# Performance work log

Measured on AMD Instinct MI355X. Metric: run time of the kernel, lower is better.

The kernel has to match this reference:

```python
import jax, jax.numpy as jnp
import numpy as np

N, D = 512, 256
NUM_CLASSES = 10
MARGIN = 1.0


def setup_inputs() -> dict:
    key = jax.random.key(0)
    k1, k2 = jax.random.split(key)
    embeddings = jax.random.normal(k1, (N, D), dtype=jnp.float32)
    labels = jax.random.randint(k2, (N,), 0, NUM_CLASSES, dtype=jnp.int32)
    return {"embeddings": embeddings, "labels": labels}


def _pairwise_euclidean(e):
    # dist[i, j] = sqrt(sum((e_i - e_j)^2)), computed via the Gram matrix.
    sq = jnp.sum(e * e, axis=-1)                       # [N]
    d2 = sq[:, None] + sq[None, :] - 2.0 * (e @ e.T)   # [N, N]
    d2 = jnp.maximum(d2, 0.0)
    # safe sqrt: zero-distance pairs (diagonal) get dist 0 with no NaN grads
    pos = d2 > 0
    return jnp.where(pos, jnp.sqrt(jnp.where(pos, d2, 1.0)), 0.0)


def reference(embeddings, labels):
    n = labels.shape[0]
    dist = _pairwise_euclidean(embeddings)             # [N, N]

    same = labels[:, None] == labels[None, :]          # [N, N]
    not_self = ~jnp.eye(n, dtype=bool)
    pos_mask = same & not_self                         # valid (anchor, positive)
    neg_mask = ~same                                   # valid (anchor, negative)

    # triplet (a, p, n): relu(d_ap - d_an + margin)
    tl = jax.nn.relu(dist[:, :, None] - dist[:, None, :] + MARGIN)  # [N, N, N]
    valid = pos_mask[:, :, None] & neg_mask[:, None, :]             # [N, N, N]

    loss_sum = jnp.sum(jnp.where(valid, tl, 0.0))
    # use_gt_than_zero_mean=False: divide by total number of valid triplets
    count = jnp.sum(valid).astype(embeddings.dtype)
    return loss_sum / count
```

## Files before the change

kernel.cpp:

```cpp
#include <hip/hip_runtime.h>

#define NN 512
#define DD 256
#define MARGIN 1.0f

__global__ __launch_bounds__(256) void triplet_partial(
    const float* __restrict__ e, const int* __restrict__ labels,
    float* __restrict__ partial, int* __restrict__ pcount)
{
    const int a    = blockIdx.x;
    const int t    = threadIdx.x;
    const int lane = t & 63;
    const int wave = t >> 6;

    __shared__ __align__(16) float ea[DD];
    __shared__ int   slab[NN];
    __shared__ float plist[NN];
    __shared__ float nlist[NN];
    __shared__ int   segP[8], segN[8];
    __shared__ float red[4];

    ea[t] = e[(size_t)a * DD + t];
    slab[t]       = labels[t];
    slab[t + 256] = labels[t + 256];
    __syncthreads();

    const int la = slab[a];

    float acc0 = 0.f, acc1 = 0.f;
    const float4* r0 = reinterpret_cast<const float4*>(e + (size_t)t * DD);
    const float4* r1 = reinterpret_cast<const float4*>(e + (size_t)(t + 256) * DD);
    #pragma unroll 4
    for (int k = 0; k < DD / 4; ++k) {
        float4 v0 = r0[k];
        float4 v1 = r1[k];
        float4 ev = *reinterpret_cast<const float4*>(&ea[k * 4]);
        float d;
        d = ev.x - v0.x; acc0 = fmaf(d, d, acc0);
        d = ev.y - v0.y; acc0 = fmaf(d, d, acc0);
        d = ev.z - v0.z; acc0 = fmaf(d, d, acc0);
        d = ev.w - v0.w; acc0 = fmaf(d, d, acc0);
        d = ev.x - v1.x; acc1 = fmaf(d, d, acc1);
        d = ev.y - v1.y; acc1 = fmaf(d, d, acc1);
        d = ev.z - v1.z; acc1 = fmaf(d, d, acc1);
        d = ev.w - v1.w; acc1 = fmaf(d, d, acc1);
    }
    const float d0 = sqrtf(acc0);
    const float d1 = sqrtf(acc1);

    const int l0 = slab[t];
    const int l1 = slab[t + 256];
    const bool vp0 = (l0 == la) && (t != a);
    const bool vp1 = (l1 == la) && (t + 256 != a);
    const bool vn0 = (l0 != la);
    const bool vn1 = (l1 != la);

    const unsigned long long mp0 = __ballot(vp0);
    const unsigned long long mp1 = __ballot(vp1);
    const unsigned long long mn0 = __ballot(vn0);
    const unsigned long long mn1 = __ballot(vn1);

    if (lane == 0) {
        segP[wave]     = __popcll(mp0);
        segP[4 + wave] = __popcll(mp1);
        segN[wave]     = __popcll(mn0);
        segN[4 + wave] = __popcll(mn1);
    }
    __syncthreads();

    int baseP0 = 0, baseP1 = 0, baseN0 = 0, baseN1 = 0, totP = 0, totN = 0;
    #pragma unroll
    for (int s = 0; s < 8; ++s) {
        const int vP = segP[s], vN = segN[s];
        totP += vP; totN += vN;
        if (s < wave)     { baseP0 += vP; baseN0 += vN; }
        if (s < 4 + wave) { baseP1 += vP; baseN1 += vN; }
    }

    const unsigned long long lower = (lane == 0) ? 0ull : ((~0ull) >> (64 - lane));
    if (vp0) plist[baseP0 + __popcll(mp0 & lower)] = d0 + MARGIN;
    if (vp1) plist[baseP1 + __popcll(mp1 & lower)] = d1 + MARGIN;
    if (vn0) nlist[baseN0 + __popcll(mn0 & lower)] = d0;
    if (vn1) nlist[baseN1 + __popcll(mn1 & lower)] = d1;
    __syncthreads();

    float sum = 0.f;
    for (int p = wave; p < totP; p += 4) {
        const float dpm = plist[p];
        for (int n = lane; n < totN; n += 64) {
            const float v = dpm - nlist[n];
            sum += fmaxf(v, 0.f);
        }
    }

    #pragma unroll
    for (int off = 32; off > 0; off >>= 1) sum += __shfl_down(sum, off);
    if (lane == 0) red[wave] = sum;
    __syncthreads();
    if (t == 0) {
        partial[a] = red[0] + red[1] + red[2] + red[3];
        pcount[a]  = totP * totN;
    }
}

__global__ __launch_bounds__(256) void reduce_final(
    const float* __restrict__ partial, const int* __restrict__ pcount,
    float* __restrict__ out)
{
    const int t = threadIdx.x;
    double s = 0.0;
    long long c = 0;
    for (int i = t; i < NN; i += 256) { s += (double)partial[i]; c += (long long)pcount[i]; }
    __shared__ double sd[256];
    __shared__ long long sc[256];
    sd[t] = s; sc[t] = c;
    __syncthreads();
    for (int off = 128; off > 0; off >>= 1) {
        if (t < off) { sd[t] += sd[t + off]; sc[t] += sc[t + off]; }
        __syncthreads();
    }
    if (t == 0) out[0] = (float)(sd[0] / (double)sc[0]);
}

extern "C" void kernel_launch(void* const* d_in, const int* in_sizes, int n_in,
                              void* d_out, int out_size, void* d_ws, size_t ws_size,
                              hipStream_t stream) {
    const float* e      = (const float*)d_in[0];
    const int*   labels = (const int*)d_in[1];
    float* out     = (float*)d_out;
    float* partial = (float*)d_ws;
    int*   pcount  = (int*)((char*)d_ws + NN * sizeof(float));

    triplet_partial<<<NN, 256, 0, stream>>>(e, labels, partial, pcount);
    reduce_final<<<1, 256, 0, stream>>>(partial, pcount, out);
}
```

Before: 92.07 us.

## Split distance computation into tiled kernel and fuse final reduction via atomics

Moves the pairwise distance computation into its own kernel in which each block computes four anchor rows against 256 columns. Each loaded embedding row is now reused across four anchors, cutting the redundant global traffic where every anchor block re-read the whole embedding matrix. The pair-counting kernel reads the precomputed distances from a workspace buffer. The separate reduction kernel is replaced by float and int atomics plus a last-block ticket that writes the output, which makes the float summation order nondeterministic and the count an int that could overflow for larger sizes.

```diff
diff --git a/kernel.cpp b/kernel.cpp
--- a/kernel.cpp
+++ b/kernel.cpp
@@ -4,49 +4,72 @@
 #define DD 256
 #define MARGIN 1.0f
 
-__global__ __launch_bounds__(256) void triplet_partial(
-    const float* __restrict__ e, const int* __restrict__ labels,
-    float* __restrict__ partial, int* __restrict__ pcount)
+__global__ __launch_bounds__(256) void dist_kernel(
+    const float* __restrict__ e, float* __restrict__ dist,
+    float* __restrict__ gsum, int* __restrict__ gcnt, int* __restrict__ gdone)
+{
+    const int g = blockIdx.x >> 1;
+    const int h = blockIdx.x & 1;
+    const int t = threadIdx.x;
+    const int j = h * 256 + t;
+    const int a0 = g * 4;
+
+    if (blockIdx.x == 0 && t == 0) { *gsum = 0.f; *gcnt = 0; *gdone = 0; }
+
+    __shared__ __align__(16) float eas[DD][4];
+
+    #pragma unroll
+    for (int ai = 0; ai < 4; ++ai)
+        eas[t][ai] = e[(size_t)(a0 + ai) * DD + t];
+    __syncthreads();
+
+    float acc0 = 0.f, acc1 = 0.f, acc2 = 0.f, acc3 = 0.f;
+    const float4* rowj = reinterpret_cast<const float4*>(e + (size_t)j * DD);
+
+    #pragma unroll 4
+    for (int kb = 0; kb < DD / 4; ++kb) {
+        const float4 v = rowj[kb];
+        const float vv[4] = {v.x, v.y, v.z, v.w};
+        #pragma unroll
+        for (int q = 0; q < 4; ++q) {
+            const float4 av = *reinterpret_cast<const float4*>(&eas[kb * 4 + q][0]);
+            float d;
+            d = av.x - vv[q]; acc0 = fmaf(d, d, acc0);
+            d = av.y - vv[q]; acc1 = fmaf(d, d, acc1);
+            d = av.z - vv[q]; acc2 = fmaf(d, d, acc2);
+            d = av.w - vv[q]; acc3 = fmaf(d, d, acc3);
+        }
+    }
+
+    dist[(size_t)(a0 + 0) * NN + j] = sqrtf(acc0);
+    dist[(size_t)(a0 + 1) * NN + j] = sqrtf(acc1);
+    dist[(size_t)(a0 + 2) * NN + j] = sqrtf(acc2);
+    dist[(size_t)(a0 + 3) * NN + j] = sqrtf(acc3);
+}
+
+__global__ __launch_bounds__(256) void pairs_kernel(
+    const float* __restrict__ dist, const int* __restrict__ labels,
+    float* __restrict__ gsum, int* __restrict__ gcnt, int* __restrict__ gdone,
+    float* __restrict__ out)
 {
     const int a    = blockIdx.x;
     const int t    = threadIdx.x;
     const int lane = t & 63;
     const int wave = t >> 6;
 
-    __shared__ __align__(16) float ea[DD];
     __shared__ int   slab[NN];
     __shared__ float plist[NN];
     __shared__ float nlist[NN];
     __shared__ int   segP[8], segN[8];
     __shared__ float red[4];
 
-    ea[t] = e[(size_t)a * DD + t];
     slab[t]       = labels[t];
     slab[t + 256] = labels[t + 256];
     __syncthreads();
 
     const int la = slab[a];
-
-    float acc0 = 0.f, acc1 = 0.f;
-    const float4* r0 = reinterpret_cast<const float4*>(e + (size_t)t * DD);
-    const float4* r1 = reinterpret_cast<const float4*>(e + (size_t)(t + 256) * DD);
-    #pragma unroll 4
-    for (int k = 0; k < DD / 4; ++k) {
-        float4 v0 = r0[k];
-        float4 v1 = r1[k];
-        float4 ev = *reinterpret_cast<const float4*>(&ea[k * 4]);
-        float d;
-        d = ev.x - v0.x; acc0 = fmaf(d, d, acc0);
-        d = ev.y - v0.y; acc0 = fmaf(d, d, acc0);
-        d = ev.z - v0.z; acc0 = fmaf(d, d, acc0);
-        d = ev.w - v0.w; acc0 = fmaf(d, d, acc0);
-        d = ev.x - v1.x; acc1 = fmaf(d, d, acc1);
-        d = ev.y - v1.y; acc1 = fmaf(d, d, acc1);
-        d = ev.z - v1.z; acc1 = fmaf(d, d, acc1);
-        d = ev.w - v1.w; acc1 = fmaf(d, d, acc1);
-    }
-    const float d0 = sqrtf(acc0);
-    const float d1 = sqrtf(acc1);
+    const float d0 = dist[(size_t)a * NN + t];
+    const float d1 = dist[(size_t)a * NN + t + 256];
 
     const int l0 = slab[t];
     const int l1 = slab[t + 256];
@@ -97,29 +120,18 @@
     for (int off = 32; off > 0; off >>= 1) sum += __shfl_down(sum, off);
     if (lane == 0) red[wave] = sum;
     __syncthreads();
+
     if (t == 0) {
-        partial[a] = red[0] + red[1] + red[2] + red[3];
-        pcount[a]  = totP * totN;
+        atomicAdd(gsum, red[0] + red[1] + red[2] + red[3]);
+        atomicAdd(gcnt, totP * totN);
+        __threadfence();
+        const int ticket = atomicAdd(gdone, 1);
+        if (ticket == NN - 1) {
+            const float s = atomicAdd(gsum, 0.0f);
+            const int   c = atomicAdd(gcnt, 0);
+            out[0] = s / (float)c;
+        }
     }
-}
-
-__global__ __launch_bounds__(256) void reduce_final(
-    const float* __restrict__ partial, const int* __restrict__ pcount,
-    float* __restrict__ out)
-{
-    const int t = threadIdx.x;
-    double s = 0.0;
-    long long c = 0;
-    for (int i = t; i < NN; i += 256) { s += (double)partial[i]; c += (long long)pcount[i]; }
-    __shared__ double sd[256];
-    __shared__ long long sc[256];
-    sd[t] = s; sc[t] = c;
-    __syncthreads();
-    for (int off = 128; off > 0; off >>= 1) {
-        if (t < off) { sd[t] += sd[t + off]; sc[t] += sc[t + off]; }
-        __syncthreads();
-    }
-    if (t == 0) out[0] = (float)(sd[0] / (double)sc[0]);
 }
 
 extern "C" void kernel_launch(void* const* d_in, const int* in_sizes, int n_in,
@@ -127,10 +139,13 @@
                               hipStream_t stream) {
     const float* e      = (const float*)d_in[0];
     const int*   labels = (const int*)d_in[1];
-    float* out     = (float*)d_out;
-    float* partial = (float*)d_ws;
-    int*   pcount  = (int*)((char*)d_ws + NN * sizeof(float));
+    float* out   = (float*)d_out;
 
-    triplet_partial<<<NN, 256, 0, stream>>>(e, labels, partial, pcount);
-    reduce_final<<<1, 256, 0, stream>>>(partial, pcount, out);
+    float* gsum  = (float*)d_ws;
+    int*   gcnt  = (int*)d_ws + 1;
+    int*   gdone = (int*)d_ws + 2;
+    float* dist  = (float*)((char*)d_ws + 256);
+
+    dist_kernel<<<256, 256, 0, stream>>>(e, dist, gsum, gcnt, gdone);
+    pairs_kernel<<<NN, 256, 0, stream>>>(dist, labels, gsum, gcnt, gdone, out);
 }
```

Result: no change. 91.08 us (-1.1%).
